# Optimization experiments

Hardware: AMD Instinct MI355X
Metric: run time of the kernel (lower is better)

## Reference

```python
import jax, jax.numpy as jnp
import numpy as np

H = 12  # num_heads

def _attn(q, k, v):
    # q,k,v: [B,H,N,D]; SDPA default scale 1/sqrt(D)
    D = q.shape[-1]
    scores = jnp.einsum('bhnd,bhmd->bhnm', q, k) / jnp.sqrt(jnp.asarray(D, q.dtype))
    p = jax.nn.softmax(scores, axis=-1)
    return jnp.einsum('bhnm,bhmd->bhnd', p, v)

def setup_inputs() -> dict:
    key = jax.random.key(0)
    ks = jax.random.split(key, 5)
    B, N, C = 2, 2048, 768
    s = 0.02
    return {
        'x': jax.random.normal(ks[0], (B, N, C), jnp.float32),
        'Wq': jax.random.normal(ks[1], (C, 2 * C), jnp.float32) * s,
        'Wk': jax.random.normal(ks[2], (C, 2 * C), jnp.float32) * s,
        'Wv': jax.random.normal(ks[3], (C, C), jnp.float32) * s,
        'lambda_p': jnp.zeros((H, 1, 1), jnp.float32),
        'Wo': jax.random.normal(ks[4], (C, C), jnp.float32) * s,
        'bo': jnp.zeros((C,), jnp.float32),
    }

def reference(x, Wq, Wk, Wv, lambda_p, Wo, bo):
    B, N, C = x.shape
    D = C // H
    # [B,N,2C] -> [2,B,H,N,D]
    q = (x @ Wq).reshape(B, N, 2, H, D).transpose(2, 0, 3, 1, 4)
    k = (x @ Wk).reshape(B, N, 2, H, D).transpose(2, 0, 3, 1, 4)
    v = (x @ Wv).reshape(B, N, H, D).transpose(0, 2, 1, 3)
    out1 = _attn(q[0], k[0], v)
    out2 = _attn(q[1], k[1], v)
    lam = jnp.exp(lambda_p)  # [H,1,1] broadcasts over [B,H,N,D]
    out = out1 - lam * out2
    out = out.transpose(0, 2, 1, 3).reshape(B, N, C)
    return out @ Wo + bo
```

## Files before the change

### kernel.cpp

```cpp
#include <hip/hip_runtime.h>

typedef unsigned short u16;
typedef unsigned int u32;
typedef unsigned long long u64;
typedef __bf16 bf16x8 __attribute__((ext_vector_type(8)));
typedef float f32x4 __attribute__((ext_vector_type(4)));

#define B_ 2
#define N_ 2048
#define C_ 768
#define H_ 12
#define M_ 4096
#define SCALE_LOG2 0.18033688011112042f

static __device__ __forceinline__ u16 f2bf(float f) {
  u32 u = __builtin_bit_cast(u32, f);
  u32 r = u + 0x7fffu + ((u >> 16) & 1u);
  return (u16)(r >> 16);
}
static __device__ __forceinline__ float fexp2(float x) {
#if __has_builtin(__builtin_amdgcn_exp2f)
  return __builtin_amdgcn_exp2f(x);
#else
  return __expf(x * 0.6931471805599453f);
#endif
}
static __device__ __forceinline__ u32 pack_bf16(float a, float b) {
  u32 r;
  asm("v_cvt_pk_bf16_f32 %0, %1, %2" : "=v"(r) : "v"(a), "v"(b));
  return r;
}
static __device__ __forceinline__ float max3f(float a, float b, float c) {
  float r;
  asm("v_max3_f32 %0, %1, %2, %3" : "=v"(r) : "v"(a), "v"(b), "v"(c));
  return r;
}

static __device__ __forceinline__ void gload16(const void* g, void* lds_base) {
  __builtin_amdgcn_global_load_lds(
      (__attribute__((address_space(1))) void*)(u64)(g),
      (__attribute__((address_space(3))) void*)(u32)(u64)(lds_base), 16, 0, 0);
}

__global__ __launch_bounds__(256) void k_cvt4(const float* __restrict__ x,
                                              u16* __restrict__ xb, int n4) {
  int i = blockIdx.x * 256 + threadIdx.x;
  if (i >= n4) return;
  float4 v = ((const float4*)x)[i];
  ushort4 o;
  o.x = f2bf(v.x); o.y = f2bf(v.y); o.z = f2bf(v.z); o.w = f2bf(v.w);
  ((ushort4*)xb)[i] = o;
}

__global__ __launch_bounds__(256) void k_tconv2(const float* __restrict__ W0,
                                                const float* __restrict__ W1,
                                                u16* __restrict__ Wt, int K, int N) {
  const float* W = blockIdx.z ? W1 : W0;
  u16* dst = Wt + (u64)blockIdx.z * N * K;
  __shared__ float t[32][33];
  int n0 = blockIdx.x * 32, k0 = blockIdx.y * 32;
  int tx = threadIdx.x, ty = threadIdx.y;
#pragma unroll
  for (int i = 0; i < 4; i++)
    t[ty + i * 8][tx] = W[(u64)(k0 + ty + i * 8) * N + n0 + tx];
  __syncthreads();
#pragma unroll
  for (int i = 0; i < 4; i++)
    dst[(u64)(n0 + ty + i * 8) * K + k0 + tx] = f2bf(t[tx][ty + i * 8]);
}

__global__ __launch_bounds__(256) void k_gemm_qkv(const u16* __restrict__ A,
                                                  const u16* __restrict__ WQK,
                                                  const u16* __restrict__ WV,
                                                  u16* __restrict__ QKb,
                                                  u16* __restrict__ Vtout) {
  __shared__ u16 As[128 * 32];
  __shared__ u16 Bs[128 * 32];
  const int t = threadIdx.x;
  const int w = t >> 6, l = t & 63;
  const int wr = w >> 1, wc = w & 1;
  const int la = l & 15, lg = l >> 4;
  const int srow = l >> 2, scb = (l & 3) << 4;
  const int by = blockIdx.y;
  const bool isV = by >= 24;

  f32x4 acc[4][4];
#pragma unroll
  for (int i = 0; i < 4; i++)
#pragma unroll
    for (int j = 0; j < 4; j++) acc[i][j] = f32x4{0.f, 0.f, 0.f, 0.f};

  const u16* Ag = A + (u64)(blockIdx.x * 128) * 768;
  const u16* Bg = isV ? WV + (u64)((by - 24) * 128) * 768 : WQK + (u64)(by * 128) * 768;

  for (int k0 = 0; k0 < 768; k0 += 32) {
#pragma unroll
    for (int j = 0; j < 2; j++) {
      int r = (w * 2 + j) * 16 + srow;
      gload16((const char*)(Ag + (u64)r * 768 + k0) + scb, (char*)As + (w * 2 + j) * 1024);
      gload16((const char*)(Bg + (u64)r * 768 + k0) + scb, (char*)Bs + (w * 2 + j) * 1024);
    }
    __syncthreads();
    bf16x8 af[4], bfr[4];
#pragma unroll
    for (int m = 0; m < 4; m++)
      af[m] = *(const bf16x8*)(As + (wr * 64 + m * 16 + la) * 32 + lg * 8);
#pragma unroll
    for (int n = 0; n < 4; n++)
      bfr[n] = *(const bf16x8*)(Bs + (wc * 64 + n * 16 + la) * 32 + lg * 8);
#pragma unroll
    for (int m = 0; m < 4; m++)
#pragma unroll
      for (int n = 0; n < 4; n++)
        acc[m][n] =
            __builtin_amdgcn_mfma_f32_16x16x32_bf16(af[m], bfr[n], acc[m][n], 0, 0, 0);
    __syncthreads();
  }

#pragma unroll
  for (int m = 0; m < 4; m++) {
#pragma unroll
    for (int n = 0; n < 4; n++) {
      int grow0 = blockIdx.x * 128 + wr * 64 + m * 16 + lg * 4;
      if (!isV) {
        int gcol = by * 128 + wc * 64 + n * 16 + la;
        float sc = (gcol < 1536) ? SCALE_LOG2 : 1.0f;
#pragma unroll
        for (int j = 0; j < 4; j++)
          QKb[(u64)(grow0 + j) * 3072 + gcol] = f2bf(acc[m][n][j] * sc);
      } else {
        int gcol = (by - 24) * 128 + wc * 64 + n * 16 + la;
        ushort4 o;
        o.x = f2bf(acc[m][n][0]); o.y = f2bf(acc[m][n][1]);
        o.z = f2bf(acc[m][n][2]); o.w = f2bf(acc[m][n][3]);
        *(ushort4*)(Vtout + (u64)gcol * M_ + grow0) = o;
      }
    }
  }
}

__global__ __launch_bounds__(256) void k_gemm_out(const u16* __restrict__ A,
                                                  const u16* __restrict__ Bt,
                                                  float* __restrict__ Cout,
                                                  const float* __restrict__ bias) {
  __shared__ u16 As[128 * 32];
  __shared__ u16 Bs[128 * 32];
  const int t = threadIdx.x;
  const int w = t >> 6, l = t & 63;
  const int wr = w >> 1, wc = w & 1;
  const int la = l & 15, lg = l >> 4;
  const int srow = l >> 2, scb = (l & 3) << 4;

  f32x4 acc[4][4];
#pragma unroll
  for (int i = 0; i < 4; i++)
#pragma unroll
    for (int j = 0; j < 4; j++) acc[i][j] = f32x4{0.f, 0.f, 0.f, 0.f};

  const u16* Ag = A + (u64)(blockIdx.x * 128) * 768;
  const u16* Bg = Bt + (u64)(blockIdx.y * 128) * 768;

  for (int k0 = 0; k0 < 768; k0 += 32) {
#pragma unroll
    for (int j = 0; j < 2; j++) {
      int r = (w * 2 + j) * 16 + srow;
      gload16((const char*)(Ag + (u64)r * 768 + k0) + scb, (char*)As + (w * 2 + j) * 1024);
      gload16((const char*)(Bg + (u64)r * 768 + k0) + scb, (char*)Bs + (w * 2 + j) * 1024);
    }
    __syncthreads();
    bf16x8 af[4], bfr[4];
#pragma unroll
    for (int m = 0; m < 4; m++)
      af[m] = *(const bf16x8*)(As + (wr * 64 + m * 16 + la) * 32 + lg * 8);
#pragma unroll
    for (int n = 0; n < 4; n++)
      bfr[n] = *(const bf16x8*)(Bs + (wc * 64 + n * 16 + la) * 32 + lg * 8);
#pragma unroll
    for (int m = 0; m < 4; m++)
#pragma unroll
      for (int n = 0; n < 4; n++)
        acc[m][n] =
            __builtin_amdgcn_mfma_f32_16x16x32_bf16(af[m], bfr[n], acc[m][n], 0, 0, 0);
    __syncthreads();
  }

#pragma unroll
  for (int m = 0; m < 4; m++) {
#pragma unroll
    for (int n = 0; n < 4; n++) {
      int grow0 = blockIdx.x * 128 + wr * 64 + m * 16 + lg * 4;
      int gcol = blockIdx.y * 128 + wc * 64 + n * 16 + la;
      float bb = bias[gcol];
#pragma unroll
      for (int j = 0; j < 4; j++)
        Cout[(u64)(grow0 + j) * 768 + gcol] = acc[m][n][j] + bb;
    }
  }
}

__global__ __launch_bounds__(512, 6) void k_attn3(const u16* __restrict__ QKb,
                                                  const u16* __restrict__ Vt,
                                                  const float* __restrict__ lamp,
                                                  u16* __restrict__ Ob) {
  const int qt = blockIdx.x, h = blockIdx.y, b = blockIdx.z;
  __shared__ __align__(16) char smem[40960];
  char* ks0 = smem;
  char* ks1 = smem + 8192;
  char* vsp = smem + 16384;
  const int t = threadIdx.x, w = t >> 6, l = t & 63;
  const int p = w >> 2, wq = w & 3;
  char* pw = smem + 24576 + w * 2048;
  const int la = l & 15, lg = l >> 4;
  const int sw2 = (la & 7) << 4;

  const u16* qrow =
      QKb + (u64)(b * N_ + qt * 64 + wq * 16 + la) * 3072 + p * 768 + h * 64 + lg * 8;
  bf16x8 q0 = *(const bf16x8*)(qrow);
  bf16x8 q1 = *(const bf16x8*)(qrow + 32);

  f32x4 oacc[4];
#pragma unroll
  for (int i = 0; i < 4; i++) oacc[i] = f32x4{0.f, 0.f, 0.f, 0.f};
  float m_run = -1e30f, l_run = 0.f;

  const int rA = t >> 3, cbs = (t & 7) << 4;
  const u32 swA = (u32)(rA * 128 + (cbs ^ ((rA & 7) << 4)));
  const char* kg = (const char*)(QKb + (u64)(b * N_ + rA) * 3072 + 1536 + h * 64) + cbs;
  const char* vg = (const char*)(Vt + (u64)(h * 64 + rA) * M_ + b * N_) + cbs;
  const u64 KSTEP = (u64)64 * 3072 * 2;

  uint4 rk0, rk1, rv;
  rk0 = *(const uint4*)(kg);
  rk1 = *(const uint4*)(kg + 1536);
  rv = *(const uint4*)(vg);

  const char* ksp = p ? ks1 : ks0;

  for (int kt = 0; kt < 32; kt++) {
    asm volatile("s_waitcnt vmcnt(0)" ::: "memory");
    __builtin_amdgcn_sched_barrier(0);
    *(uint4*)(ks0 + swA) = rk0;
    *(uint4*)(ks1 + swA) = rk1;
    *(uint4*)(vsp + swA) = rv;
    asm volatile("s_waitcnt lgkmcnt(0)" ::: "memory");
    __builtin_amdgcn_s_barrier();
    kg += KSTEP;
    vg += 128;
    if (kt < 31) {
      rk0 = *(const uint4*)(kg);
      rk1 = *(const uint4*)(kg + 1536);
      rv = *(const uint4*)(vg);
    }
    __builtin_amdgcn_sched_barrier(0);

    f32x4 st[4];
#pragma unroll
    for (int c = 0; c < 4; c++) {
      int row = c * 16 + la;
      int sw = (row & 7) << 4;
      bf16x8 kf0 = *(const bf16x8*)(ksp + row * 128 + ((lg * 16) ^ sw));
      bf16x8 kf1 = *(const bf16x8*)(ksp + row * 128 + ((64 + lg * 16) ^ sw));
      f32x4 z = f32x4{0.f, 0.f, 0.f, 0.f};
      z = __builtin_amdgcn_mfma_f32_16x16x32_bf16(kf0, q0, z, 0, 0, 0);
      z = __builtin_amdgcn_mfma_f32_16x16x32_bf16(kf1, q1, z, 0, 0, 0);
      st[c] = z;
    }
    float m0 = max3f(st[0][0], st[0][1], st[0][2]);
    float m1 = max3f(st[0][3], st[1][0], st[1][1]);
    float m2 = max3f(st[1][2], st[1][3], st[2][0]);
    float m3 = max3f(st[2][1], st[2][2], st[2][3]);
    float m4 = max3f(st[3][0], st[3][1], st[3][2]);
    float pmax = fmaxf(max3f(m0, m1, m2), max3f(m3, m4, st[3][3]));
    pmax = fmaxf(pmax, __shfl_xor(pmax, 16, 64));
    pmax = fmaxf(pmax, __shfl_xor(pmax, 32, 64));
    if (__any(pmax - m_run > 8.f)) {
      float mnew = fmaxf(m_run, pmax);
      float corr = fexp2(m_run - mnew);
      l_run *= corr;
      float cT0 = __shfl(corr, lg * 4 + 0, 64);
      float cT1 = __shfl(corr, lg * 4 + 1, 64);
      float cT2 = __shfl(corr, lg * 4 + 2, 64);
      float cT3 = __shfl(corr, lg * 4 + 3, 64);
#pragma unroll
      for (int cd = 0; cd < 4; cd++) {
        oacc[cd][0] *= cT0;
        oacc[cd][1] *= cT1;
        oacc[cd][2] *= cT2;
        oacc[cd][3] *= cT3;
      }
      m_run = mnew;
    }
    float ls = 0.f;
#pragma unroll
    for (int c = 0; c < 4; c++)
#pragma unroll
      for (int j = 0; j < 4; j++) {
        float e = fexp2(st[c][j] - m_run);
        st[c][j] = e;
        ls += e;
      }
    ls += __shfl_xor(ls, 16, 64);
    ls += __shfl_xor(ls, 32, 64);
    l_run += ls;
#pragma unroll
    for (int c = 0; c < 4; c++) {
      uint2 pr;
      pr.x = pack_bf16(st[c][0], st[c][1]);
      pr.y = pack_bf16(st[c][2], st[c][3]);
      int kvb = c * 32 + lg * 8;
      *(uint2*)(pw + la * 128 + (kvb ^ sw2)) = pr;
    }
    bf16x8 pf0 = *(const bf16x8*)(pw + la * 128 + ((lg * 16) ^ sw2));
    bf16x8 pf1 = *(const bf16x8*)(pw + la * 128 + ((64 + lg * 16) ^ sw2));
#pragma unroll
    for (int cd = 0; cd < 4; cd++) {
      int row = cd * 16 + la;
      int sw = (row & 7) << 4;
      bf16x8 v0 = *(const bf16x8*)(vsp + row * 128 + ((lg * 16) ^ sw));
      bf16x8 v1 = *(const bf16x8*)(vsp + row * 128 + ((64 + lg * 16) ^ sw));
      oacc[cd] = __builtin_amdgcn_mfma_f32_16x16x32_bf16(pf0, v0, oacc[cd], 0, 0, 0);
      oacc[cd] = __builtin_amdgcn_mfma_f32_16x16x32_bf16(pf1, v1, oacc[cd], 0, 0, 0);
    }
    __builtin_amdgcn_s_barrier();
  }

  float inv = 1.f / l_run;
  float s0 = __shfl(inv, lg * 4 + 0, 64);
  float s1 = __shfl(inv, lg * 4 + 1, 64);
  float s2 = __shfl(inv, lg * 4 + 2, 64);
  float s3 = __shfl(inv, lg * 4 + 3, 64);
  float sj[4] = {s0, s1, s2, s3};
  float* cmb = (float*)smem + wq * (16 * 66);
  __syncthreads();
  if (p == 1) {
    float lam = __expf(lamp[h]);
#pragma unroll
    for (int cd = 0; cd < 4; cd++)
#pragma unroll
      for (int j = 0; j < 4; j++)
        cmb[(lg * 4 + j) * 66 + cd * 16 + la] = lam * oacc[cd][j] * sj[j];
  }
  __syncthreads();
  if (p == 0) {
    u16* Og = Ob + (u64)(b * N_ + qt * 64 + wq * 16) * C_ + h * 64;
#pragma unroll
    for (int cd = 0; cd < 4; cd++)
#pragma unroll
      for (int j = 0; j < 4; j++) {
        float v = oacc[cd][j] * sj[j] - cmb[(lg * 4 + j) * 66 + cd * 16 + la];
        Og[(u64)(lg * 4 + j) * C_ + cd * 16 + la] = f2bf(v);
      }
  }
}

extern "C" void kernel_launch(void* const* d_in, const int* in_sizes, int n_in,
                              void* d_out, int out_size, void* d_ws, size_t ws_size,
                              hipStream_t stream) {
  const float* x = (const float*)d_in[0];
  const float* Wq = (const float*)d_in[1];
  const float* Wk = (const float*)d_in[2];
  const float* Wv = (const float*)d_in[3];
  const float* lamp = (const float*)d_in[4];
  const float* Wo = (const float*)d_in[5];
  const float* bo = (const float*)d_in[6];

  char* ws = (char*)d_ws;
  u16* xb = (u16*)ws;    ws += (u64)M_ * C_ * 2;
  u16* wqkt = (u16*)ws;  ws += (u64)4 * C_ * C_ * 2;
  u16* wvo = (u16*)ws;   ws += (u64)2 * C_ * C_ * 2;
  u16* QKb = (u16*)ws;   ws += (u64)M_ * 4 * C_ * 2;
  u16* Vt = (u16*)ws;    ws += (u64)C_ * M_ * 2;
  u16* Ob = (u16*)ws;    ws += (u64)M_ * C_ * 2;
  u16* wvt = wvo;
  u16* wot = wvo + (u64)C_ * C_;

  k_cvt4<<<dim3(M_ * C_ / 4 / 256), 256, 0, stream>>>(x, xb, M_ * C_ / 4);
  k_tconv2<<<dim3(48, 24, 2), dim3(32, 8), 0, stream>>>(Wq, Wk, wqkt, 768, 1536);
  k_tconv2<<<dim3(24, 24, 2), dim3(32, 8), 0, stream>>>(Wv, Wo, wvo, 768, 768);
  k_gemm_qkv<<<dim3(32, 30), 256, 0, stream>>>(xb, wqkt, wvt, QKb, Vt);
  k_attn3<<<dim3(32, 12, 2), 512, 0, stream>>>(QKb, Vt, lamp, Ob);
  k_gemm_out<<<dim3(32, 6), 256, 0, stream>>>(Ob, wot, (float*)d_out, bo);
}
```

Before: 154.5 us.

## Rewrite attention kernel with 32x32 MFMA tiles, 4 waves, and XCD-aware block mapping

The attention kernel moves from 8 waves with 16x16x32 MFMAs to 4 waves of 256 threads, each computing a 32-query by 64-key tile with 32x32x16 MFMAs. Each thread now stages twice as many K/V rows per iteration. The launch becomes a 1D grid whose block index is remapped so that blocks sharing a head and batch sit on the same XCD, which is meant to improve L2 reuse of K/V. The goal is fewer LDS fragment reads per MFMA and less reduction overhead per row, in exchange for more registers per thread (launch bounds 256,3) and fewer waves per CU.

```diff
diff --git a/kernel.cpp b/kernel.cpp
--- a/kernel.cpp
+++ b/kernel.cpp
@@ -5,6 +5,7 @@
 typedef unsigned long long u64;
 typedef __bf16 bf16x8 __attribute__((ext_vector_type(8)));
 typedef float f32x4 __attribute__((ext_vector_type(4)));
+typedef float f32x16 __attribute__((ext_vector_type(16)));
 
 #define B_ 2
 #define N_ 2048
@@ -28,11 +29,6 @@
 static __device__ __forceinline__ u32 pack_bf16(float a, float b) {
   u32 r;
   asm("v_cvt_pk_bf16_f32 %0, %1, %2" : "=v"(r) : "v"(a), "v"(b));
-  return r;
-}
-static __device__ __forceinline__ float max3f(float a, float b, float c) {
-  float r;
-  asm("v_max3_f32 %0, %1, %2, %3" : "=v"(r) : "v"(a), "v"(b), "v"(c));
   return r;
 }
 
@@ -198,158 +194,177 @@
   }
 }
 
-__global__ __launch_bounds__(512, 6) void k_attn3(const u16* __restrict__ QKb,
+__global__ __launch_bounds__(256, 3) void k_attn5(const u16* __restrict__ QKb,
                                                   const u16* __restrict__ Vt,
                                                   const float* __restrict__ lamp,
                                                   u16* __restrict__ Ob) {
-  const int qt = blockIdx.x, h = blockIdx.y, b = blockIdx.z;
+  const int hw = blockIdx.x;
+  const int wid = (hw & 7) * 96 + (hw >> 3);
+  const int qt = wid & 31;
+  const int hb = wid >> 5;
+  const int h = hb % H_, b = hb / H_;
+
   __shared__ __align__(16) char smem[40960];
   char* ks0 = smem;
   char* ks1 = smem + 8192;
   char* vsp = smem + 16384;
   const int t = threadIdx.x, w = t >> 6, l = t & 63;
-  const int p = w >> 2, wq = w & 3;
-  char* pw = smem + 24576 + w * 2048;
-  const int la = l & 15, lg = l >> 4;
-  const int sw2 = (la & 7) << 4;
+  const int p = w >> 1, s = w & 1;
+  const int ql = l & 31, hh = l >> 5;
+  char* pw = smem + 24576 + w * 4096;
+  const int swq = (ql & 7) << 4;
 
   const u16* qrow =
-      QKb + (u64)(b * N_ + qt * 64 + wq * 16 + la) * 3072 + p * 768 + h * 64 + lg * 8;
-  bf16x8 q0 = *(const bf16x8*)(qrow);
-  bf16x8 q1 = *(const bf16x8*)(qrow + 32);
-
-  f32x4 oacc[4];
-#pragma unroll
-  for (int i = 0; i < 4; i++) oacc[i] = f32x4{0.f, 0.f, 0.f, 0.f};
+      QKb + (u64)(b * N_ + qt * 64 + s * 32 + ql) * 3072 + p * 768 + h * 64 + hh * 8;
+  bf16x8 qf[4];
+#pragma unroll
+  for (int c = 0; c < 4; c++) qf[c] = *(const bf16x8*)(qrow + 16 * c);
+
+  f32x16 oacc0, oacc1;
+#pragma unroll
+  for (int r = 0; r < 16; r++) { oacc0[r] = 0.f; oacc1[r] = 0.f; }
   float m_run = -1e30f, l_run = 0.f;
 
   const int rA = t >> 3, cbs = (t & 7) << 4;
   const u32 swA = (u32)(rA * 128 + (cbs ^ ((rA & 7) << 4)));
   const char* kg = (const char*)(QKb + (u64)(b * N_ + rA) * 3072 + 1536 + h * 64) + cbs;
   const char* vg = (const char*)(Vt + (u64)(h * 64 + rA) * M_ + b * N_) + cbs;
+  const u64 KR32 = (u64)32 * 3072 * 2;
+  const u64 VR32 = (u64)32 * M_ * 2;
   const u64 KSTEP = (u64)64 * 3072 * 2;
 
-  uint4 rk0, rk1, rv;
-  rk0 = *(const uint4*)(kg);
-  rk1 = *(const uint4*)(kg + 1536);
-  rv = *(const uint4*)(vg);
+  uint4 rk0A, rk0B, rk1A, rk1B, rvA, rvB;
+#define LOADS6()                              \
+  do {                                        \
+    rk0A = *(const uint4*)(kg);               \
+    rk0B = *(const uint4*)(kg + KR32);        \
+    rk1A = *(const uint4*)(kg + 1536);        \
+    rk1B = *(const uint4*)(kg + 1536 + KR32); \
+    rvA = *(const uint4*)(vg);                \
+    rvB = *(const uint4*)(vg + VR32);         \
+  } while (0)
+  LOADS6();
 
   const char* ksp = p ? ks1 : ks0;
+  int koff[4];
+#pragma unroll
+  for (int c = 0; c < 4; c++) koff[c] = (32 * c + 16 * hh) ^ swq;
 
   for (int kt = 0; kt < 32; kt++) {
     asm volatile("s_waitcnt vmcnt(0)" ::: "memory");
     __builtin_amdgcn_sched_barrier(0);
-    *(uint4*)(ks0 + swA) = rk0;
-    *(uint4*)(ks1 + swA) = rk1;
-    *(uint4*)(vsp + swA) = rv;
+    *(uint4*)(ks0 + swA) = rk0A;
+    *(uint4*)(ks0 + swA + 4096) = rk0B;
+    *(uint4*)(ks1 + swA) = rk1A;
+    *(uint4*)(ks1 + swA + 4096) = rk1B;
+    *(uint4*)(vsp + swA) = rvA;
+    *(uint4*)(vsp + swA + 4096) = rvB;
     asm volatile("s_waitcnt lgkmcnt(0)" ::: "memory");
     __builtin_amdgcn_s_barrier();
     kg += KSTEP;
     vg += 128;
-    if (kt < 31) {
-      rk0 = *(const uint4*)(kg);
-      rk1 = *(const uint4*)(kg + 1536);
-      rv = *(const uint4*)(vg);
-    }
+    if (kt < 31) LOADS6();
     __builtin_amdgcn_sched_barrier(0);
 
-    f32x4 st[4];
+    f32x16 st0, st1;
+#pragma unroll
+    for (int r = 0; r < 16; r++) { st0[r] = 0.f; st1[r] = 0.f; }
 #pragma unroll
     for (int c = 0; c < 4; c++) {
-      int row = c * 16 + la;
-      int sw = (row & 7) << 4;
-      bf16x8 kf0 = *(const bf16x8*)(ksp + row * 128 + ((lg * 16) ^ sw));
-      bf16x8 kf1 = *(const bf16x8*)(ksp + row * 128 + ((64 + lg * 16) ^ sw));
-      f32x4 z = f32x4{0.f, 0.f, 0.f, 0.f};
-      z = __builtin_amdgcn_mfma_f32_16x16x32_bf16(kf0, q0, z, 0, 0, 0);
-      z = __builtin_amdgcn_mfma_f32_16x16x32_bf16(kf1, q1, z, 0, 0, 0);
-      st[c] = z;
-    }
-    float m0 = max3f(st[0][0], st[0][1], st[0][2]);
-    float m1 = max3f(st[0][3], st[1][0], st[1][1]);
-    float m2 = max3f(st[1][2], st[1][3], st[2][0]);
-    float m3 = max3f(st[2][1], st[2][2], st[2][3]);
-    float m4 = max3f(st[3][0], st[3][1], st[3][2]);
-    float pmax = fmaxf(max3f(m0, m1, m2), max3f(m3, m4, st[3][3]));
-    pmax = fmaxf(pmax, __shfl_xor(pmax, 16, 64));
-    pmax = fmaxf(pmax, __shfl_xor(pmax, 32, 64));
+      bf16x8 kf0 = *(const bf16x8*)(ksp + ql * 128 + koff[c]);
+      bf16x8 kf1 = *(const bf16x8*)(ksp + (32 + ql) * 128 + koff[c]);
+      st0 = __builtin_amdgcn_mfma_f32_32x32x16_bf16(kf0, qf[c], st0, 0, 0, 0);
+      st1 = __builtin_amdgcn_mfma_f32_32x32x16_bf16(kf1, qf[c], st1, 0, 0, 0);
+    }
+
+    float mx[16];
+#pragma unroll
+    for (int r = 0; r < 16; r++) mx[r] = fmaxf(st0[r], st1[r]);
+#pragma unroll
+    for (int sd = 8; sd >= 1; sd >>= 1)
+#pragma unroll
+      for (int r = 0; r < sd; r++) mx[r] = fmaxf(mx[r], mx[r + sd]);
+    float pmax = fmaxf(mx[0], __shfl_xor(mx[0], 32, 64));
+
     if (__any(pmax - m_run > 8.f)) {
       float mnew = fmaxf(m_run, pmax);
       float corr = fexp2(m_run - mnew);
       l_run *= corr;
-      float cT0 = __shfl(corr, lg * 4 + 0, 64);
-      float cT1 = __shfl(corr, lg * 4 + 1, 64);
-      float cT2 = __shfl(corr, lg * 4 + 2, 64);
-      float cT3 = __shfl(corr, lg * 4 + 3, 64);
-#pragma unroll
-      for (int cd = 0; cd < 4; cd++) {
-        oacc[cd][0] *= cT0;
-        oacc[cd][1] *= cT1;
-        oacc[cd][2] *= cT2;
-        oacc[cd][3] *= cT3;
-      }
+      float cT[16];
+#pragma unroll
+      for (int r = 0; r < 16; r++)
+        cT[r] = __shfl(corr, (r & 3) + 8 * (r >> 2) + 4 * hh, 64);
+#pragma unroll
+      for (int r = 0; r < 16; r++) { oacc0[r] *= cT[r]; oacc1[r] *= cT[r]; }
       m_run = mnew;
     }
-    float ls = 0.f;
+#pragma unroll
+    for (int r = 0; r < 16; r++) {
+      st0[r] = fexp2(st0[r] - m_run);
+      st1[r] = fexp2(st1[r] - m_run);
+    }
+    float sm[16];
+#pragma unroll
+    for (int r = 0; r < 16; r++) sm[r] = st0[r] + st1[r];
+#pragma unroll
+    for (int sd = 8; sd >= 1; sd >>= 1)
+#pragma unroll
+      for (int r = 0; r < sd; r++) sm[r] += sm[r + sd];
+    l_run += sm[0] + __shfl_xor(sm[0], 32, 64);
+
+#pragma unroll
+    for (int g = 0; g < 4; g++) {
+      uint2 w0, w1;
+      w0.x = pack_bf16(st0[4 * g + 0], st0[4 * g + 1]);
+      w0.y = pack_bf16(st0[4 * g + 2], st0[4 * g + 3]);
+      w1.x = pack_bf16(st1[4 * g + 0], st1[4 * g + 1]);
+      w1.y = pack_bf16(st1[4 * g + 2], st1[4 * g + 3]);
+      int bo = 16 * g + 8 * hh;
+      *(uint2*)(pw + ql * 128 + (bo ^ swq)) = w0;
+      *(uint2*)(pw + ql * 128 + ((64 + bo) ^ swq)) = w1;
+    }
+    bf16x8 pa[4];
 #pragma unroll
     for (int c = 0; c < 4; c++)
-#pragma unroll
-      for (int j = 0; j < 4; j++) {
-        float e = fexp2(st[c][j] - m_run);
-        st[c][j] = e;
-        ls += e;
-      }
-    ls += __shfl_xor(ls, 16, 64);
-    ls += __shfl_xor(ls, 32, 64);
-    l_run += ls;
+      pa[c] = *(const bf16x8*)(pw + ql * 128 + koff[c]);
+
 #pragma unroll
     for (int c = 0; c < 4; c++) {
-      uint2 pr;
-      pr.x = pack_bf16(st[c][0], st[c][1]);
-      pr.y = pack_bf16(st[c][2], st[c][3]);
-      int kvb = c * 32 + lg * 8;
-      *(uint2*)(pw + la * 128 + (kvb ^ sw2)) = pr;
-    }
-    bf16x8 pf0 = *(const bf16x8*)(pw + la * 128 + ((lg * 16) ^ sw2));
-    bf16x8 pf1 = *(const bf16x8*)(pw + la * 128 + ((64 + lg * 16) ^ sw2));
-#pragma unroll
-    for (int cd = 0; cd < 4; cd++) {
-      int row = cd * 16 + la;
-      int sw = (row & 7) << 4;
-      bf16x8 v0 = *(const bf16x8*)(vsp + row * 128 + ((lg * 16) ^ sw));
-      bf16x8 v1 = *(const bf16x8*)(vsp + row * 128 + ((64 + lg * 16) ^ sw));
-      oacc[cd] = __builtin_amdgcn_mfma_f32_16x16x32_bf16(pf0, v0, oacc[cd], 0, 0, 0);
-      oacc[cd] = __builtin_amdgcn_mfma_f32_16x16x32_bf16(pf1, v1, oacc[cd], 0, 0, 0);
+      bf16x8 vf0 = *(const bf16x8*)(vsp + ql * 128 + koff[c]);
+      bf16x8 vf1 = *(const bf16x8*)(vsp + (32 + ql) * 128 + koff[c]);
+      oacc0 = __builtin_amdgcn_mfma_f32_32x32x16_bf16(pa[c], vf0, oacc0, 0, 0, 0);
+      oacc1 = __builtin_amdgcn_mfma_f32_32x32x16_bf16(pa[c], vf1, oacc1, 0, 0, 0);
     }
     __builtin_amdgcn_s_barrier();
   }
 
   float inv = 1.f / l_run;
-  float s0 = __shfl(inv, lg * 4 + 0, 64);
-  float s1 = __shfl(inv, lg * 4 + 1, 64);
-  float s2 = __shfl(inv, lg * 4 + 2, 64);
-  float s3 = __shfl(inv, lg * 4 + 3, 64);
-  float sj[4] = {s0, s1, s2, s3};
-  float* cmb = (float*)smem + wq * (16 * 66);
+  float iT[16];
+#pragma unroll
+  for (int r = 0; r < 16; r++)
+    iT[r] = __shfl(inv, (r & 3) + 8 * (r >> 2) + 4 * hh, 64);
+  float* cmb = (float*)smem;
   __syncthreads();
   if (p == 1) {
     float lam = __expf(lamp[h]);
 #pragma unroll
-    for (int cd = 0; cd < 4; cd++)
-#pragma unroll
-      for (int j = 0; j < 4; j++)
-        cmb[(lg * 4 + j) * 66 + cd * 16 + la] = lam * oacc[cd][j] * sj[j];
+    for (int r = 0; r < 16; r++) {
+      int qr = (r & 3) + 8 * (r >> 2) + 4 * hh;
+      cmb[(s * 32 + qr) * 64 + ql] = lam * oacc0[r] * iT[r];
+      cmb[(s * 32 + qr) * 64 + 32 + ql] = lam * oacc1[r] * iT[r];
+    }
   }
   __syncthreads();
   if (p == 0) {
-    u16* Og = Ob + (u64)(b * N_ + qt * 64 + wq * 16) * C_ + h * 64;
-#pragma unroll
-    for (int cd = 0; cd < 4; cd++)
-#pragma unroll
-      for (int j = 0; j < 4; j++) {
-        float v = oacc[cd][j] * sj[j] - cmb[(lg * 4 + j) * 66 + cd * 16 + la];
-        Og[(u64)(lg * 4 + j) * C_ + cd * 16 + la] = f2bf(v);
-      }
+    u16* Og = Ob + (u64)(b * N_ + qt * 64 + s * 32) * C_ + h * 64;
+#pragma unroll
+    for (int r = 0; r < 16; r++) {
+      int qr = (r & 3) + 8 * (r >> 2) + 4 * hh;
+      float v0 = oacc0[r] * iT[r] - cmb[(s * 32 + qr) * 64 + ql];
+      float v1 = oacc1[r] * iT[r] - cmb[(s * 32 + qr) * 64 + 32 + ql];
+      Og[(u64)qr * C_ + ql] = f2bf(v0);
+      Og[(u64)qr * C_ + 32 + ql] = f2bf(v1);
+    }
   }
 }
 
@@ -378,6 +393,6 @@
   k_tconv2<<<dim3(48, 24, 2), dim3(32, 8), 0, stream>>>(Wq, Wk, wqkt, 768, 1536);
   k_tconv2<<<dim3(24, 24, 2), dim3(32, 8), 0, stream>>>(Wv, Wo, wvo, 768, 768);
   k_gemm_qkv<<<dim3(32, 30), 256, 0, stream>>>(xb, wqkt, wvt, QKb, Vt);
-  k_attn3<<<dim3(32, 12, 2), 512, 0, stream>>>(QKb, Vt, lamp, Ob);
+  k_attn5<<<dim3(768), 256, 0, stream>>>(QKb, Vt, lamp, Ob);
   k_gemm_out<<<dim3(32, 6), 256, 0, stream>>>(Ob, wot, (float*)d_out, bo);
 }
```

New measurement: 152.0 us. Within noise of the previous version (-1.6%).
